# Kernel optimization log

Measured on AMD Instinct MI355X. Metric: run time of the kernel, lower is better.

Reference implementation:

```python
import jax, jax.numpy as jnp
import numpy as np

B, T, C, H = 8, 2048, 1024, 64


def setup_inputs() -> dict:
    key = jax.random.key(0)
    kx, kq, kk, kv = jax.random.split(key, 4)
    sc = 1.0 / np.sqrt(C)
    return {
        "x": jax.random.normal(kx, (B, T, C), dtype=jnp.float32),
        "Wq": jax.random.normal(kq, (C, H), dtype=jnp.float32) * sc,
        "Wk": jax.random.normal(kk, (C, H), dtype=jnp.float32) * sc,
        "Wv": jax.random.normal(kv, (C, H), dtype=jnp.float32) * sc,
    }


def reference(x, Wq, Wk, Wv):
    # Projections: Linear(C, head_size, bias=False) == x @ W
    q = jnp.einsum("btc,ch->bth", x, Wq)
    k = jnp.einsum("btc,ch->bth", x, Wk)
    v = jnp.einsum("btc,ch->bth", x, Wv)
    head_size = q.shape[-1]
    scale = head_size ** -0.5
    # scores: [B, T, T]
    scores = jnp.einsum("bqh,bkh->bqk", q, k) * scale
    # causal mask (tril==0 -> -inf)
    causal = jnp.tril(jnp.ones((scores.shape[1], scores.shape[2]), dtype=bool))
    scores = jnp.where(causal, scores, -jnp.inf)
    w = jax.nn.softmax(scores, axis=-1)
    # dropout_rate=0.0 -> identity
    out = jnp.einsum("bqk,bkh->bqh", w, v)
    return out
```

## Files before the change

kernel.cpp:

```cpp
#include <hip/hip_runtime.h>
#include <hip/hip_bf16.h>
#include <cstdint>
#include <cstddef>

typedef short bf16x8 __attribute__((ext_vector_type(8)));
typedef float f32x4 __attribute__((ext_vector_type(4)));

#define BN 8
#define TN 2048
#define CN 1024
#define HN 64

__device__ __forceinline__ unsigned short f2bf(float f) {
    unsigned int u = __float_as_uint(f);
    u += 0x7fffu + ((u >> 16) & 1u);
    return (unsigned short)(u >> 16);
}

__device__ __forceinline__ int pk2(float lo, float hi) {
    float2 t; t.x = lo; t.y = hi;
    __hip_bfloat162 h = __float22bfloat162_rn(t);
    return *reinterpret_cast<int*>(&h);
}

__device__ __forceinline__ void gload_lds16(const unsigned short* gsrc, void* ldst) {
    __builtin_amdgcn_global_load_lds(
        (const __attribute__((address_space(1))) unsigned int*)gsrc,
        (__attribute__((address_space(3))) unsigned int*)ldst,
        16, 0, 0);
}

__global__ __launch_bounds__(256) void wconv_kernel(const float* __restrict__ Wq,
                                                    const float* __restrict__ Wk,
                                                    const float* __restrict__ Wv,
                                                    unsigned short* __restrict__ Wp) {
    int idx = blockIdx.x * 256 + threadIdx.x;
    int n = idx >> 10;
    int c = idx & 1023;
    int m = n >> 6;
    int h = n & 63;
    const float* W = (m == 0) ? Wq : ((m == 1) ? Wk : Wv);
    float v = W[c * 64 + h];
    if (m == 0) v *= 0.18033688011112042f;
    const int tile = n >> 4, lq = n & 15;
    const int kk = c >> 5, lg = (c >> 3) & 3, e = c & 7;
    Wp[(size_t)(((tile * 32 + kk) * 64 + lg * 16 + lq) * 8 + e)] = f2bf(v);
}

__global__ __launch_bounds__(512) void proj_kernel(const float* __restrict__ X,
                                                   const unsigned short* __restrict__ Wp,
                                                   unsigned short* __restrict__ Qs,
                                                   unsigned short* __restrict__ Kp,
                                                   unsigned short* __restrict__ Vp) {
    __shared__ short Xs[2][32 * 64];
    __shared__ short Wsh[2][12288];

    const int tid = threadIdx.x;
    const int w   = tid >> 6;
    const int l   = tid & 63;
    const int lq  = l & 15;
    const int lg  = l >> 4;
    const int wr  = w >> 2;
    const int wc  = w & 3;
    const int rowbase = blockIdx.x * 32;

    const int xrow = tid >> 4;
    const int xcol = (tid & 15) * 4;
    const float* xsrc = X + (size_t)(rowbase + xrow) * CN + xcol;
    const int xdst = xrow * 128 + (((tid & 15) * 8) ^ ((xrow & 7) << 4));

    const unsigned short* wsrc[3];
    int wbase[3];
    #pragma unroll
    for (int j = 0; j < 3; ++j) {
        const int el  = j * 4096 + tid * 8;
        const int blk = el >> 9;
        const int t   = blk >> 1, kkL = blk & 1;
        wsrc[j]  = Wp + (t * 32 + kkL) * 512 + (el & 511);
        wbase[j] = j * 4096 + w * 512;
    }

    const int arow = wr * 16 + lq;
    int aaddr[2];
    #pragma unroll
    for (int kkL = 0; kkL < 2; ++kkL)
        aaddr[kkL] = arow * 128 + (((kkL * 64 + lg * 16)) ^ ((arow & 7) << 4));
    int baddr[2][3];
    #pragma unroll
    for (int kkL = 0; kkL < 2; ++kkL)
        #pragma unroll
        for (int jj = 0; jj < 3; ++jj)
            baddr[kkL][jj] = (((wc * 3 + jj) * 2 + kkL) * 64 + l) * 16;

    const f32x4 zero4 = {0.f, 0.f, 0.f, 0.f};
    f32x4 acc[3] = {zero4, zero4, zero4};

    {
        #pragma unroll
        for (int j = 0; j < 3; ++j)
            gload_lds16(wsrc[j], (char*)Wsh[0] + wbase[j] * 2);
        float4 xr = *(const float4*)(xsrc);
        int2 xc; xc.x = pk2(xr.x, xr.y); xc.y = pk2(xr.z, xr.w);
        *(int2*)((char*)Xs[0] + xdst) = xc;
        __syncthreads();
    }

    for (int s = 0; s < 16; ++s) {
        const int cur = s & 1;
        const int nxt = cur ^ 1;
        const bool more = (s + 1) < 16;
        float4 xr;
        if (more) {
            #pragma unroll
            for (int j = 0; j < 3; ++j)
                gload_lds16(wsrc[j] + (s + 1) * 1024, (char*)Wsh[nxt] + wbase[j] * 2);
            xr = *(const float4*)(xsrc + (s + 1) * 64);
        }
        #pragma unroll
        for (int kkL = 0; kkL < 2; ++kkL) {
            bf16x8 a  = *(const bf16x8*)((char*)Xs[cur] + aaddr[kkL]);
            bf16x8 b0 = *(const bf16x8*)((char*)Wsh[cur] + baddr[kkL][0]);
            bf16x8 b1 = *(const bf16x8*)((char*)Wsh[cur] + baddr[kkL][1]);
            bf16x8 b2 = *(const bf16x8*)((char*)Wsh[cur] + baddr[kkL][2]);
            acc[0] = __builtin_amdgcn_mfma_f32_16x16x32_bf16(a, b0, acc[0], 0, 0, 0);
            acc[1] = __builtin_amdgcn_mfma_f32_16x16x32_bf16(a, b1, acc[1], 0, 0, 0);
            acc[2] = __builtin_amdgcn_mfma_f32_16x16x32_bf16(a, b2, acc[2], 0, 0, 0);
        }
        if (more) {
            int2 xc; xc.x = pk2(xr.x, xr.y); xc.y = pk2(xr.z, xr.w);
            *(int2*)((char*)Xs[nxt] + xdst) = xc;
        }
        __syncthreads();
    }

    #pragma unroll
    for (int j = 0; j < 3; ++j) {
        const int col = wc * 48 + j * 16 + lq;
        const int mtx = col >> 6;
        const int h   = col & 63;
        #pragma unroll
        for (int i = 0; i < 4; ++i) {
            const int g = rowbase + wr * 16 + 4 * lg + i;
            const unsigned short val = f2bf(acc[j][i]);
            const int b = g >> 11, tloc = g & 2047;
            const int kt = tloc >> 5;
            if (mtx == 0) {
                Qs[(size_t)g * 64 + h] = val;
            } else if (mtx == 1) {
                const int fa = (tloc >> 4) & 1, lqk = tloc & 15;
                const int ks = h >> 5, lgk = (h >> 3) & 3, e = h & 7;
                Kp[(size_t)(b * 64 + kt) * 2048 + (fa * 2 + ks) * 512 +
                   (lgk * 16 + lqk) * 8 + e] = val;
            } else {
                const int tt = tloc & 31;
                const int lgv = (tt & 15) >> 2;
                const int e = (tt < 16) ? (tt & 3) : 4 + (tt & 3);
                const int nf = h >> 4, lqv = h & 15;
                Vp[(size_t)(b * 64 + kt) * 2048 + nf * 512 +
                   (lgv * 16 + lqv) * 8 + e] = val;
            }
        }
    }
}

__global__ __launch_bounds__(256) void attn_kernel(const unsigned short* __restrict__ Qs,
                                                   const unsigned short* __restrict__ Kp,
                                                   const unsigned short* __restrict__ Vp,
                                                   float* __restrict__ Out) {
    __shared__ float lm[4][16];
    __shared__ float ll[4][16];
    __shared__ float facc[4][1024];

    const int tid = threadIdx.x;
    const int w  = tid >> 6;
    const int l  = tid & 63;
    const int lq = l & 15;
    const int lg = l >> 4;
    const int bid = blockIdx.x;
    const int qt = 127 - (bid >> 3);
    const int b  = bid & 7;
    const int q0 = qt * 16;
    const int nt = (qt >> 1) + 1;

    const unsigned short* Qb = Qs + (size_t)b * TN * 64;
    const unsigned short* KVbase_k = Kp + (size_t)b * 64 * 2048 + (size_t)l * 8;
    const unsigned short* KVbase_v = Vp + (size_t)b * 64 * 2048 + (size_t)l * 8;

    const f32x4 zero4 = {0.f, 0.f, 0.f, 0.f};

    bf16x8 qa0 = *(const bf16x8*)(Qb + (size_t)(q0 + lq) * 64 + lg * 8);
    bf16x8 qa1 = *(const bf16x8*)(Qb + (size_t)(q0 + lq) * 64 + 32 + lg * 8);

    f32x4 acc[4] = {zero4, zero4, zero4, zero4};
    float mrow = -1e30f;
    float lrow = 0.f;

    bf16x8 Kc[4], Vc[4], Kn[4], Vn[4];
    int kt = w;
    if (kt < nt) {
        const size_t tb = (size_t)kt * 2048;
        #pragma unroll
        for (int i = 0; i < 4; ++i) {
            Kc[i] = *(const bf16x8*)(KVbase_k + tb + i * 512);
            Vc[i] = *(const bf16x8*)(KVbase_v + tb + i * 512);
        }
    }

    for (; kt < nt; kt += 4) {
        const int ktn = kt + 4;
        if (ktn < nt) {
            const size_t tb = (size_t)ktn * 2048;
            #pragma unroll
            for (int i = 0; i < 4; ++i) {
                Kn[i] = *(const bf16x8*)(KVbase_k + tb + i * 512);
                Vn[i] = *(const bf16x8*)(KVbase_v + tb + i * 512);
            }
        }

        const int key0 = kt * 32;
        f32x4 s[2];
        s[0] = __builtin_amdgcn_mfma_f32_16x16x32_bf16(Kc[0], qa0, zero4, 0, 0, 0);
        s[0] = __builtin_amdgcn_mfma_f32_16x16x32_bf16(Kc[1], qa1, s[0], 0, 0, 0);
        s[1] = __builtin_amdgcn_mfma_f32_16x16x32_bf16(Kc[2], qa0, zero4, 0, 0, 0);
        s[1] = __builtin_amdgcn_mfma_f32_16x16x32_bf16(Kc[3], qa1, s[1], 0, 0, 0);

        if (kt == nt - 1) {
            const int q = q0 + lq;
            #pragma unroll
            for (int fa = 0; fa < 2; ++fa)
                #pragma unroll
                for (int r = 0; r < 4; ++r) {
                    const int key = key0 + fa * 16 + 4 * lg + r;
                    if (key > q) s[fa][r] = -1e30f;
                }
        }

        float m1 = fmaxf(fmaxf(s[0][0], s[0][1]), s[0][2]);
        float m2 = fmaxf(fmaxf(s[0][3], s[1][0]), s[1][1]);
        float m3 = fmaxf(fmaxf(s[1][2], s[1][3]), m1);
        float tm = fmaxf(m2, m3);
        tm = fmaxf(tm, __shfl_xor(tm, 16));
        tm = fmaxf(tm, __shfl_xor(tm, 32));

        if (!__all(tm <= mrow + 8.0f)) {
            const float mnew = fmaxf(mrow, tm);
            const float cc = __builtin_amdgcn_exp2f(mrow - mnew);
            lrow *= cc;
            float cb[4];
            #pragma unroll
            for (int i = 0; i < 4; ++i) cb[i] = __shfl(cc, 4 * lg + i);
            #pragma unroll
            for (int nf = 0; nf < 4; ++nf)
                #pragma unroll
                for (int i = 0; i < 4; ++i) acc[nf][i] *= cb[i];
            mrow = mnew;
        }

        float p[2][4];
        float psum = 0.f;
        #pragma unroll
        for (int fa = 0; fa < 2; ++fa)
            #pragma unroll
            for (int r = 0; r < 4; ++r) {
                p[fa][r] = __builtin_amdgcn_exp2f(s[fa][r] - mrow);
                psum += p[fa][r];
            }
        psum += __shfl_xor(psum, 16);
        psum += __shfl_xor(psum, 32);
        lrow += psum;

        bf16x8 pa;
        pa[0] = (short)f2bf(p[0][0]); pa[1] = (short)f2bf(p[0][1]);
        pa[2] = (short)f2bf(p[0][2]); pa[3] = (short)f2bf(p[0][3]);
        pa[4] = (short)f2bf(p[1][0]); pa[5] = (short)f2bf(p[1][1]);
        pa[6] = (short)f2bf(p[1][2]); pa[7] = (short)f2bf(p[1][3]);

        acc[0] = __builtin_amdgcn_mfma_f32_16x16x32_bf16(pa, Vc[0], acc[0], 0, 0, 0);
        acc[1] = __builtin_amdgcn_mfma_f32_16x16x32_bf16(pa, Vc[1], acc[1], 0, 0, 0);
        acc[2] = __builtin_amdgcn_mfma_f32_16x16x32_bf16(pa, Vc[2], acc[2], 0, 0, 0);
        acc[3] = __builtin_amdgcn_mfma_f32_16x16x32_bf16(pa, Vc[3], acc[3], 0, 0, 0);

        #pragma unroll
        for (int i = 0; i < 4; ++i) { Kc[i] = Kn[i]; Vc[i] = Vn[i]; }
    }

    if (lg == 0) {
        lm[w][lq] = mrow;
        ll[w][lq] = lrow;
    }
    #pragma unroll
    for (int nf = 0; nf < 4; ++nf)
        #pragma unroll
        for (int i = 0; i < 4; ++i)
            facc[w][(4 * lg + i) * 64 + nf * 16 + lq] = acc[nf][i];

    __syncthreads();

    #pragma unroll
    for (int ii = 0; ii < 4; ++ii) {
        const int e = tid + ii * 256;
        const int q = e >> 6;
        const int h = e & 63;
        const float M = fmaxf(fmaxf(lm[0][q], lm[1][q]),
                              fmaxf(lm[2][q], lm[3][q]));
        float L = 0.f, O = 0.f;
        #pragma unroll
        for (int c = 0; c < 4; ++c) {
            const float wgt = __builtin_amdgcn_exp2f(lm[c][q] - M);
            L += wgt * ll[c][q];
            O += wgt * facc[c][q * 64 + h];
        }
        Out[((size_t)b * TN + q0 + q) * 64 + h] = O / L;
    }
}

extern "C" void kernel_launch(void* const* d_in, const int* in_sizes, int n_in,
                              void* d_out, int out_size, void* d_ws, size_t ws_size,
                              hipStream_t stream) {
    const float* X  = (const float*)d_in[0];
    const float* Wq = (const float*)d_in[1];
    const float* Wk = (const float*)d_in[2];
    const float* Wv = (const float*)d_in[3];
    float* Out = (float*)d_out;

    char* ws = (char*)d_ws;
    unsigned short* Wp = (unsigned short*)(ws);
    unsigned short* Qs = (unsigned short*)(ws + (512u << 10));
    unsigned short* Kp = Qs + (size_t)16384 * 64;
    unsigned short* Vp = Kp + (size_t)16384 * 64;

    hipLaunchKernelGGL(wconv_kernel, dim3(768), dim3(256), 0, stream, Wq, Wk, Wv, Wp);
    hipLaunchKernelGGL(proj_kernel,  dim3(512), dim3(512), 0, stream, X, Wp, Qs, Kp, Vp);
    hipLaunchKernelGGL(attn_kernel,  dim3(1024), dim3(256), 0, stream, Qs, Kp, Vp, Out);
}
```

Measured before the change: 42.51 us.

## Retile projection GEMM to 64-row by 96-column blocks split across two N halves

Each projection block previously computed 32 rows by all 192 output columns (Q, K and V). It now computes 64 rows by 96 columns, and the grid is split into two N halves using a 256-tile M index plus an N-half index. This halves the weight tile staged in LDS per block, doubles the X rows loaded per block, and moves X loads to 8 floats per thread. The intent is to rebalance X versus W reuse and change block count and occupancy. In exchange, each X row is now read from global memory by two blocks instead of one.

```diff
diff --git a/kernel.cpp b/kernel.cpp
--- a/kernel.cpp
+++ b/kernel.cpp
@@ -52,35 +52,32 @@
                                                    unsigned short* __restrict__ Qs,
                                                    unsigned short* __restrict__ Kp,
                                                    unsigned short* __restrict__ Vp) {
-    __shared__ short Xs[2][32 * 64];
-    __shared__ short Wsh[2][12288];
+    __shared__ short Xs[2][64 * 64];
+    __shared__ short Wsh[2][6144];
 
     const int tid = threadIdx.x;
     const int w   = tid >> 6;
     const int l   = tid & 63;
     const int lq  = l & 15;
     const int lg  = l >> 4;
-    const int wr  = w >> 2;
-    const int wc  = w & 3;
-    const int rowbase = blockIdx.x * 32;
-
-    const int xrow = tid >> 4;
-    const int xcol = (tid & 15) * 4;
+    const int mr   = w >> 1;
+    const int nsub = w & 1;
+    const int bid = blockIdx.x;
+    const int mtile = bid & 255;
+    const int nh    = bid >> 8;
+    const int rowbase = mtile * 64;
+
+    const int xrow = tid >> 3;
+    const int xcol = (tid & 7) * 8;
     const float* xsrc = X + (size_t)(rowbase + xrow) * CN + xcol;
-    const int xdst = xrow * 128 + (((tid & 15) * 8) ^ ((xrow & 7) << 4));
-
-    const unsigned short* wsrc[3];
-    int wbase[3];
-    #pragma unroll
-    for (int j = 0; j < 3; ++j) {
-        const int el  = j * 4096 + tid * 8;
-        const int blk = el >> 9;
-        const int t   = blk >> 1, kkL = blk & 1;
-        wsrc[j]  = Wp + (t * 32 + kkL) * 512 + (el & 511);
-        wbase[j] = j * 4096 + w * 512;
-    }
-
-    const int arow = wr * 16 + lq;
+    const int xdst = xrow * 128 + (((xcol * 2)) ^ ((xrow & 7) << 4));
+
+    const unsigned short* wsrc0 = Wp + (size_t)((nh * 6 + (w >> 1)) * 32 + (w & 1)) * 512 + l * 8;
+    const int wdstb0 = (w * 512) * 2;
+    const unsigned short* wsrc1 = Wp + (size_t)((nh * 6 + 4 + (w >> 1)) * 32 + (w & 1)) * 512 + l * 8;
+    const int wdstb1 = (4096 + w * 512) * 2;
+
+    const int arow = mr * 16 + lq;
     int aaddr[2];
     #pragma unroll
     for (int kkL = 0; kkL < 2; ++kkL)
@@ -90,18 +87,20 @@
     for (int kkL = 0; kkL < 2; ++kkL)
         #pragma unroll
         for (int jj = 0; jj < 3; ++jj)
-            baddr[kkL][jj] = (((wc * 3 + jj) * 2 + kkL) * 64 + l) * 16;
+            baddr[kkL][jj] = (((nsub * 3 + jj) * 2 + kkL) * 512 + l * 8) * 2;
 
     const f32x4 zero4 = {0.f, 0.f, 0.f, 0.f};
     f32x4 acc[3] = {zero4, zero4, zero4};
 
     {
-        #pragma unroll
-        for (int j = 0; j < 3; ++j)
-            gload_lds16(wsrc[j], (char*)Wsh[0] + wbase[j] * 2);
-        float4 xr = *(const float4*)(xsrc);
-        int2 xc; xc.x = pk2(xr.x, xr.y); xc.y = pk2(xr.z, xr.w);
-        *(int2*)((char*)Xs[0] + xdst) = xc;
+        gload_lds16(wsrc0, (char*)Wsh[0] + wdstb0);
+        if (tid < 256) gload_lds16(wsrc1, (char*)Wsh[0] + wdstb1);
+        float4 xa = *(const float4*)(xsrc);
+        float4 xb = *(const float4*)(xsrc + 4);
+        int4 xc;
+        xc.x = pk2(xa.x, xa.y); xc.y = pk2(xa.z, xa.w);
+        xc.z = pk2(xb.x, xb.y); xc.w = pk2(xb.z, xb.w);
+        *(int4*)((char*)Xs[0] + xdst) = xc;
         __syncthreads();
     }
 
@@ -109,12 +108,12 @@
         const int cur = s & 1;
         const int nxt = cur ^ 1;
         const bool more = (s + 1) < 16;
-        float4 xr;
+        float4 xa, xb;
         if (more) {
-            #pragma unroll
-            for (int j = 0; j < 3; ++j)
-                gload_lds16(wsrc[j] + (s + 1) * 1024, (char*)Wsh[nxt] + wbase[j] * 2);
-            xr = *(const float4*)(xsrc + (s + 1) * 64);
+            xa = *(const float4*)(xsrc + (s + 1) * 64);
+            xb = *(const float4*)(xsrc + (s + 1) * 64 + 4);
+            gload_lds16(wsrc0 + (s + 1) * 1024, (char*)Wsh[nxt] + wdstb0);
+            if (tid < 256) gload_lds16(wsrc1 + (s + 1) * 1024, (char*)Wsh[nxt] + wdstb1);
         }
         #pragma unroll
         for (int kkL = 0; kkL < 2; ++kkL) {
@@ -127,21 +126,23 @@
             acc[2] = __builtin_amdgcn_mfma_f32_16x16x32_bf16(a, b2, acc[2], 0, 0, 0);
         }
         if (more) {
-            int2 xc; xc.x = pk2(xr.x, xr.y); xc.y = pk2(xr.z, xr.w);
-            *(int2*)((char*)Xs[nxt] + xdst) = xc;
+            int4 xc;
+            xc.x = pk2(xa.x, xa.y); xc.y = pk2(xa.z, xa.w);
+            xc.z = pk2(xb.x, xb.y); xc.w = pk2(xb.z, xb.w);
+            *(int4*)((char*)Xs[nxt] + xdst) = xc;
         }
         __syncthreads();
     }
 
     #pragma unroll
-    for (int j = 0; j < 3; ++j) {
-        const int col = wc * 48 + j * 16 + lq;
+    for (int jj = 0; jj < 3; ++jj) {
+        const int col = nh * 96 + nsub * 48 + jj * 16 + lq;
         const int mtx = col >> 6;
         const int h   = col & 63;
         #pragma unroll
         for (int i = 0; i < 4; ++i) {
-            const int g = rowbase + wr * 16 + 4 * lg + i;
-            const unsigned short val = f2bf(acc[j][i]);
+            const int g = rowbase + mr * 16 + 4 * lg + i;
+            const unsigned short val = f2bf(acc[jj][i]);
             const int b = g >> 11, tloc = g & 2047;
             const int kt = tloc >> 5;
             if (mtx == 0) {
```

Result: no change. 43.25 us (+1.8%).

## Process two 16-row query tiles per attention block to reuse K/V loads

Applied to the files above, without the earlier changes.

Each attention block now handles 32 query rows (two 16-row tiles) instead of 16, so every K/V fragment loaded from global memory feeds two QK and PV MFMA chains. The grid is halved to 512 blocks and the shared-memory merge buffers are doubled. The aim is to halve K/V global traffic per query and add independent MFMA work for latency hiding. The cost is more register pressure, larger LDS use, fewer blocks for load balancing, and some wasted masked work on the diagonal tile.

```diff
diff --git a/kernel.cpp b/kernel.cpp
--- a/kernel.cpp
+++ b/kernel.cpp
@@ -65,8 +65,7 @@
     const int rowbase = blockIdx.x * 32;
 
     const int xrow = tid >> 4;
-    const int xcol = (tid & 15) * 4;
-    const float* xsrc = X + (size_t)(rowbase + xrow) * CN + xcol;
+    const float* xsrc = X + (size_t)(rowbase + xrow) * CN + (tid & 15) * 4;
     const int xdst = xrow * 128 + (((tid & 15) * 8) ^ ((xrow & 7) << 4));
 
     const unsigned short* wsrc[3];
@@ -167,9 +166,9 @@
                                                    const unsigned short* __restrict__ Kp,
                                                    const unsigned short* __restrict__ Vp,
                                                    float* __restrict__ Out) {
-    __shared__ float lm[4][16];
-    __shared__ float ll[4][16];
-    __shared__ float facc[4][1024];
+    __shared__ float lm[2][4][16];
+    __shared__ float ll[2][4][16];
+    __shared__ float facc[2][4][1024];
 
     const int tid = threadIdx.x;
     const int w  = tid >> 6;
@@ -177,10 +176,11 @@
     const int lq = l & 15;
     const int lg = l >> 4;
     const int bid = blockIdx.x;
-    const int qt = 127 - (bid >> 3);
+    const int a  = 63 - (bid >> 3);
     const int b  = bid & 7;
-    const int q0 = qt * 16;
-    const int nt = (qt >> 1) + 1;
+    const int nt = a + 1;
+    const int q00 = 32 * a;
+    const int q01 = 32 * a + 16;
 
     const unsigned short* Qb = Qs + (size_t)b * TN * 64;
     const unsigned short* KVbase_k = Kp + (size_t)b * 64 * 2048 + (size_t)l * 8;
@@ -188,12 +188,15 @@
 
     const f32x4 zero4 = {0.f, 0.f, 0.f, 0.f};
 
-    bf16x8 qa0 = *(const bf16x8*)(Qb + (size_t)(q0 + lq) * 64 + lg * 8);
-    bf16x8 qa1 = *(const bf16x8*)(Qb + (size_t)(q0 + lq) * 64 + 32 + lg * 8);
-
-    f32x4 acc[4] = {zero4, zero4, zero4, zero4};
-    float mrow = -1e30f;
-    float lrow = 0.f;
+    bf16x8 qa00 = *(const bf16x8*)(Qb + (size_t)(q00 + lq) * 64 + lg * 8);
+    bf16x8 qa10 = *(const bf16x8*)(Qb + (size_t)(q00 + lq) * 64 + 32 + lg * 8);
+    bf16x8 qa01 = *(const bf16x8*)(Qb + (size_t)(q01 + lq) * 64 + lg * 8);
+    bf16x8 qa11 = *(const bf16x8*)(Qb + (size_t)(q01 + lq) * 64 + 32 + lg * 8);
+
+    f32x4 acc0[4] = {zero4, zero4, zero4, zero4};
+    f32x4 acc1[4] = {zero4, zero4, zero4, zero4};
+    float mrow0 = -1e30f, lrow0 = 0.f;
+    float mrow1 = -1e30f, lrow1 = 0.f;
 
     bf16x8 Kc[4], Vc[4], Kn[4], Vn[4];
     int kt = w;
@@ -205,6 +208,50 @@
             Vc[i] = *(const bf16x8*)(KVbase_v + tb + i * 512);
         }
     }
+
+    #define SOFTMAX_PV(S, MROW, LROW, ACC)                                        \
+        do {                                                                      \
+            float m1 = fmaxf(fmaxf(S[0][0], S[0][1]), S[0][2]);                   \
+            float m2 = fmaxf(fmaxf(S[0][3], S[1][0]), S[1][1]);                   \
+            float m3 = fmaxf(fmaxf(S[1][2], S[1][3]), m1);                        \
+            float tm = fmaxf(m2, m3);                                             \
+            tm = fmaxf(tm, __shfl_xor(tm, 16));                                   \
+            tm = fmaxf(tm, __shfl_xor(tm, 32));                                   \
+            if (!__all(tm <= MROW + 8.0f)) {                                      \
+                const float mnew = fmaxf(MROW, tm);                               \
+                const float cc = __builtin_amdgcn_exp2f(MROW - mnew);             \
+                LROW *= cc;                                                       \
+                float cb[4];                                                      \
+                _Pragma("unroll")                                                 \
+                for (int i = 0; i < 4; ++i) cb[i] = __shfl(cc, 4 * lg + i);       \
+                _Pragma("unroll")                                                 \
+                for (int nf = 0; nf < 4; ++nf)                                    \
+                    _Pragma("unroll")                                             \
+                    for (int i = 0; i < 4; ++i) ACC[nf][i] *= cb[i];              \
+                MROW = mnew;                                                      \
+            }                                                                     \
+            float p[2][4];                                                        \
+            float psum = 0.f;                                                     \
+            _Pragma("unroll")                                                     \
+            for (int fa = 0; fa < 2; ++fa)                                        \
+                _Pragma("unroll")                                                 \
+                for (int r = 0; r < 4; ++r) {                                     \
+                    p[fa][r] = __builtin_amdgcn_exp2f(S[fa][r] - MROW);           \
+                    psum += p[fa][r];                                             \
+                }                                                                 \
+            psum += __shfl_xor(psum, 16);                                         \
+            psum += __shfl_xor(psum, 32);                                         \
+            LROW += psum;                                                         \
+            bf16x8 pa;                                                            \
+            pa[0] = (short)f2bf(p[0][0]); pa[1] = (short)f2bf(p[0][1]);           \
+            pa[2] = (short)f2bf(p[0][2]); pa[3] = (short)f2bf(p[0][3]);           \
+            pa[4] = (short)f2bf(p[1][0]); pa[5] = (short)f2bf(p[1][1]);           \
+            pa[6] = (short)f2bf(p[1][2]); pa[7] = (short)f2bf(p[1][3]);           \
+            ACC[0] = __builtin_amdgcn_mfma_f32_16x16x32_bf16(pa, Vc[0], ACC[0], 0, 0, 0); \
+            ACC[1] = __builtin_amdgcn_mfma_f32_16x16x32_bf16(pa, Vc[1], ACC[1], 0, 0, 0); \
+            ACC[2] = __builtin_amdgcn_mfma_f32_16x16x32_bf16(pa, Vc[2], ACC[2], 0, 0, 0); \
+            ACC[3] = __builtin_amdgcn_mfma_f32_16x16x32_bf16(pa, Vc[3], ACC[3], 0, 0, 0); \
+        } while (0)
 
     for (; kt < nt; kt += 4) {
         const int ktn = kt + 4;
@@ -218,99 +265,70 @@
         }
 
         const int key0 = kt * 32;
-        f32x4 s[2];
-        s[0] = __builtin_amdgcn_mfma_f32_16x16x32_bf16(Kc[0], qa0, zero4, 0, 0, 0);
-        s[0] = __builtin_amdgcn_mfma_f32_16x16x32_bf16(Kc[1], qa1, s[0], 0, 0, 0);
-        s[1] = __builtin_amdgcn_mfma_f32_16x16x32_bf16(Kc[2], qa0, zero4, 0, 0, 0);
-        s[1] = __builtin_amdgcn_mfma_f32_16x16x32_bf16(Kc[3], qa1, s[1], 0, 0, 0);
+        f32x4 s0[2], s1[2];
+        s0[0] = __builtin_amdgcn_mfma_f32_16x16x32_bf16(Kc[0], qa00, zero4, 0, 0, 0);
+        s0[0] = __builtin_amdgcn_mfma_f32_16x16x32_bf16(Kc[1], qa10, s0[0], 0, 0, 0);
+        s0[1] = __builtin_amdgcn_mfma_f32_16x16x32_bf16(Kc[2], qa00, zero4, 0, 0, 0);
+        s0[1] = __builtin_amdgcn_mfma_f32_16x16x32_bf16(Kc[3], qa10, s0[1], 0, 0, 0);
+        s1[0] = __builtin_amdgcn_mfma_f32_16x16x32_bf16(Kc[0], qa01, zero4, 0, 0, 0);
+        s1[0] = __builtin_amdgcn_mfma_f32_16x16x32_bf16(Kc[1], qa11, s1[0], 0, 0, 0);
+        s1[1] = __builtin_amdgcn_mfma_f32_16x16x32_bf16(Kc[2], qa01, zero4, 0, 0, 0);
+        s1[1] = __builtin_amdgcn_mfma_f32_16x16x32_bf16(Kc[3], qa11, s1[1], 0, 0, 0);
 
         if (kt == nt - 1) {
-            const int q = q0 + lq;
+            const int qg0 = q00 + lq;
+            const int qg1 = q01 + lq;
             #pragma unroll
             for (int fa = 0; fa < 2; ++fa)
                 #pragma unroll
                 for (int r = 0; r < 4; ++r) {
                     const int key = key0 + fa * 16 + 4 * lg + r;
-                    if (key > q) s[fa][r] = -1e30f;
+                    if (key > qg0) s0[fa][r] = -1e30f;
+                    if (key > qg1) s1[fa][r] = -1e30f;
                 }
         }
 
-        float m1 = fmaxf(fmaxf(s[0][0], s[0][1]), s[0][2]);
-        float m2 = fmaxf(fmaxf(s[0][3], s[1][0]), s[1][1]);
-        float m3 = fmaxf(fmaxf(s[1][2], s[1][3]), m1);
-        float tm = fmaxf(m2, m3);
-        tm = fmaxf(tm, __shfl_xor(tm, 16));
-        tm = fmaxf(tm, __shfl_xor(tm, 32));
-
-        if (!__all(tm <= mrow + 8.0f)) {
-            const float mnew = fmaxf(mrow, tm);
-            const float cc = __builtin_amdgcn_exp2f(mrow - mnew);
-            lrow *= cc;
-            float cb[4];
+        SOFTMAX_PV(s0, mrow0, lrow0, acc0);
+        SOFTMAX_PV(s1, mrow1, lrow1, acc1);
+
+        #pragma unroll
+        for (int i = 0; i < 4; ++i) { Kc[i] = Kn[i]; Vc[i] = Vn[i]; }
+    }
+    #undef SOFTMAX_PV
+
+    if (lg == 0) {
+        lm[0][w][lq] = mrow0;  ll[0][w][lq] = lrow0;
+        lm[1][w][lq] = mrow1;  ll[1][w][lq] = lrow1;
+    }
+    #pragma unroll
+    for (int nf = 0; nf < 4; ++nf)
+        #pragma unroll
+        for (int i = 0; i < 4; ++i) {
+            facc[0][w][(4 * lg + i) * 64 + nf * 16 + lq] = acc0[nf][i];
+            facc[1][w][(4 * lg + i) * 64 + nf * 16 + lq] = acc1[nf][i];
+        }
+
+    __syncthreads();
+
+    #pragma unroll
+    for (int hh = 0; hh < 2; ++hh) {
+        const int q0 = (hh == 0) ? q00 : q01;
+        #pragma unroll
+        for (int ii = 0; ii < 4; ++ii) {
+            const int e = tid + ii * 256;
+            const int q = e >> 6;
+            const int h = e & 63;
+            const float M = fmaxf(fmaxf(lm[hh][0][q], lm[hh][1][q]),
+                                  fmaxf(lm[hh][2][q], lm[hh][3][q]));
+            float L = 0.f, O = 0.f;
             #pragma unroll
-            for (int i = 0; i < 4; ++i) cb[i] = __shfl(cc, 4 * lg + i);
-            #pragma unroll
-            for (int nf = 0; nf < 4; ++nf)
-                #pragma unroll
-                for (int i = 0; i < 4; ++i) acc[nf][i] *= cb[i];
-            mrow = mnew;
-        }
-
-        float p[2][4];
-        float psum = 0.f;
-        #pragma unroll
-        for (int fa = 0; fa < 2; ++fa)
-            #pragma unroll
-            for (int r = 0; r < 4; ++r) {
-                p[fa][r] = __builtin_amdgcn_exp2f(s[fa][r] - mrow);
-                psum += p[fa][r];
+            for (int c = 0; c < 4; ++c) {
+                const float wgt = __builtin_amdgcn_exp2f(lm[hh][c][q] - M);
+                L += wgt * ll[hh][c][q];
+                O += wgt * facc[hh][c][q * 64 + h];
             }
-        psum += __shfl_xor(psum, 16);
-        psum += __shfl_xor(psum, 32);
-        lrow += psum;
-
-        bf16x8 pa;
-        pa[0] = (short)f2bf(p[0][0]); pa[1] = (short)f2bf(p[0][1]);
-        pa[2] = (short)f2bf(p[0][2]); pa[3] = (short)f2bf(p[0][3]);
-        pa[4] = (short)f2bf(p[1][0]); pa[5] = (short)f2bf(p[1][1]);
-        pa[6] = (short)f2bf(p[1][2]); pa[7] = (short)f2bf(p[1][3]);
-
-        acc[0] = __builtin_amdgcn_mfma_f32_16x16x32_bf16(pa, Vc[0], acc[0], 0, 0, 0);
-        acc[1] = __builtin_amdgcn_mfma_f32_16x16x32_bf16(pa, Vc[1], acc[1], 0, 0, 0);
-        acc[2] = __builtin_amdgcn_mfma_f32_16x16x32_bf16(pa, Vc[2], acc[2], 0, 0, 0);
-        acc[3] = __builtin_amdgcn_mfma_f32_16x16x32_bf16(pa, Vc[3], acc[3], 0, 0, 0);
-
-        #pragma unroll
-        for (int i = 0; i < 4; ++i) { Kc[i] = Kn[i]; Vc[i] = Vn[i]; }
-    }
-
-    if (lg == 0) {
-        lm[w][lq] = mrow;
-        ll[w][lq] = lrow;
-    }
-    #pragma unroll
-    for (int nf = 0; nf < 4; ++nf)
-        #pragma unroll
-        for (int i = 0; i < 4; ++i)
-            facc[w][(4 * lg + i) * 64 + nf * 16 + lq] = acc[nf][i];
-
-    __syncthreads();
-
-    #pragma unroll
-    for (int ii = 0; ii < 4; ++ii) {
-        const int e = tid + ii * 256;
-        const int q = e >> 6;
-        const int h = e & 63;
-        const float M = fmaxf(fmaxf(lm[0][q], lm[1][q]),
-                              fmaxf(lm[2][q], lm[3][q]));
-        float L = 0.f, O = 0.f;
-        #pragma unroll
-        for (int c = 0; c < 4; ++c) {
-            const float wgt = __builtin_amdgcn_exp2f(lm[c][q] - M);
-            L += wgt * ll[c][q];
-            O += wgt * facc[c][q * 64 + h];
-        }
-        Out[((size_t)b * TN + q0 + q) * 64 + h] = O / L;
+            Out[((size_t)b * TN + q0 + q) * 64 + h] = O / L;
+        }
     }
 }
 
@@ -331,5 +349,5 @@
 
     hipLaunchKernelGGL(wconv_kernel, dim3(768), dim3(256), 0, stream, Wq, Wk, Wv, Wp);
     hipLaunchKernelGGL(proj_kernel,  dim3(512), dim3(512), 0, stream, X, Wp, Qs, Kp, Vp);
-    hipLaunchKernelGGL(attn_kernel,  dim3(1024), dim3(256), 0, stream, Qs, Kp, Vp, Out);
-}
+    hipLaunchKernelGGL(attn_kernel,  dim3(512), dim3(256), 0, stream, Qs, Kp, Vp, Out);
+}
```

Result: slower. 46.80 us (+10.1%).
